# Kernel optimization log

Measured on AMD Instinct MI355X. Metric: run time of the kernel, lower is better.

Reference implementation:

```python
import jax, jax.numpy as jnp
import numpy as np

EPS = 1e-5
K = 3

def _bn(x, g, b):
    # training-mode BatchNorm2d: batch stats over (N,H,W), biased variance
    m = jnp.mean(x, axis=(0, 2, 3), keepdims=True)
    v = jnp.var(x, axis=(0, 2, 3), keepdims=True)
    return (x - m) * jax.lax.rsqrt(v + EPS) * g[None, :, None, None] + b[None, :, None, None]

def _gelu(x):
    return jax.nn.gelu(x, approximate=False)

def _dyn_dw(x, aw1, ab1, aw2, ab2):
    # dynamic depthwise conv: per-sample k^2 softmax weights shared over channels
    b, c, h, w = x.shape
    gap = jnp.mean(x, axis=(2, 3))                              # (b,c)
    h1 = jax.nn.relu(jnp.einsum('oc,bc->bo', aw1, gap) + ab1)   # (b,c//8)
    kw = jax.nn.softmax(jnp.einsum('oc,bc->bo', aw2, h1) + ab2, axis=1)  # (b,k^2)
    xp = jnp.pad(x, ((0, 0), (0, 0), (1, 1), (1, 1)))
    out = jnp.zeros_like(x)
    idx = 0
    for i in range(K):
        for j in range(K):
            out = out + kw[:, idx, None, None, None] * xp[:, :, i:i + h, j:j + w]
            idx += 1
    return out

def _channel_att(x, w1, w2):
    avg = jnp.mean(x, axis=(2, 3))        # (b,C)
    mx = jnp.max(x, axis=(2, 3))          # (b,C)
    def fc(v):
        return jnp.einsum('oc,bc->bo', w2, jax.nn.relu(jnp.einsum('oc,bc->bo', w1, v)))
    s = jax.nn.sigmoid(fc(avg) + fc(mx))  # (b,C)
    return s[:, :, None, None] * x

def _forward(x, w1, b1, g1, be1, aw1, ab1, aw2, ab2, g2, be2,
             ca_w1, ca_w2, pw, pb, g3, be3, sw, sb):
    b, n, d = x.shape
    h = w = int(np.sqrt(n))
    residual = x
    xi = jnp.transpose(x.reshape(b, h, w, d), (0, 3, 1, 2))       # (b,d,h,w)
    # pw_expand: 1x1 conv -> GELU -> BN
    y = jnp.einsum('oc,bchw->bohw', w1, xi) + b1[None, :, None, None]
    y = _bn(_gelu(y), g1, be1)                                    # (b,4d,h,w)
    # dw_conv: dynamic depthwise -> GELU -> BN -> channel attention
    y = _dyn_dw(y, aw1, ab1, aw2, ab2)
    y = _bn(_gelu(y), g2, be2)
    y = _channel_att(y, ca_w1, ca_w2)
    # spatial attention
    avg_o = jnp.mean(y, axis=1, keepdims=True)
    max_o = jnp.max(y, axis=1, keepdims=True)
    sp_in = jnp.concatenate([avg_o, max_o], axis=1)               # (b,2,h,w)
    sp = jax.lax.conv_general_dilated(sp_in, sw, (1, 1), ((3, 3), (3, 3)),
                                      dimension_numbers=('NCHW', 'OIHW', 'NCHW'))
    sp = jax.nn.sigmoid(sp + sb[None, :, None, None])
    y = y * sp
    # pw_project: 1x1 conv -> BN
    y = jnp.einsum('oc,bchw->bohw', pw, y) + pb[None, :, None, None]
    y = _bn(y, g3, be3)
    y = jnp.transpose(y, (0, 2, 3, 1)).reshape(b, n, d)
    return residual + y

def setup_inputs() -> dict:
    key = jax.random.key(0)
    ks = jax.random.split(key, 16)
    d, C = 256, 1024
    def rn(k, shape, fan):
        return jax.random.normal(k, shape, jnp.float32) * np.float32(np.sqrt(2.0 / fan))
    return {
        'x': jax.random.normal(ks[0], (8, 1024, d), jnp.float32),
        'w1': rn(ks[1], (C, d), d), 'b1': jnp.zeros((C,), jnp.float32),
        'g1': jnp.ones((C,), jnp.float32), 'be1': jnp.zeros((C,), jnp.float32),
        'aw1': rn(ks[2], (C // 8, C), C), 'ab1': jnp.zeros((C // 8,), jnp.float32),
        'aw2': rn(ks[3], (K * K, C // 8), C // 8), 'ab2': jnp.zeros((K * K,), jnp.float32),
        'g2': jnp.ones((C,), jnp.float32), 'be2': jnp.zeros((C,), jnp.float32),
        'ca_w1': rn(ks[4], (C // 16, C), C), 'ca_w2': rn(ks[5], (C, C // 16), C // 16),
        'pw': rn(ks[6], (d, C), C), 'pb': jnp.zeros((d,), jnp.float32),
        'g3': jnp.ones((d,), jnp.float32), 'be3': jnp.zeros((d,), jnp.float32),
        'sw': rn(ks[7], (1, 2, 7, 7), 2 * 49), 'sb': jnp.zeros((1,), jnp.float32),
    }

def reference(x, w1, b1, g1, be1, aw1, ab1, aw2, ab2, g2, be2,
              ca_w1, ca_w2, pw, pb, g3, be3, sw, sb):
    return _forward(x, w1, b1, g1, be1, aw1, ab1, aw2, ab2, g2, be2,
                    ca_w1, ca_w2, pw, pb, g3, be3, sw, sb)
```

## Files before the change

kernel.cpp:

```cpp
#include <hip/hip_runtime.h>
#include <math.h>

constexpr int B = 8;
constexpr int D = 256;
constexpr int C = 1024;
constexpr int H = 32, W = 32;
constexpr int P = H * W;
constexpr int M = B * P;
constexpr float EPS = 1e-5f;

typedef unsigned short u16;
typedef unsigned int u32;
typedef __attribute__((ext_vector_type(8))) short short8;
typedef __attribute__((ext_vector_type(4))) float floatx4;

constexpr size_t WS_CHSUM1 = 0;
constexpr size_t WS_CHSQ1  = 1024;
constexpr size_t WS_GAPSUM = 2048;
constexpr size_t WS_CHSUM3 = 10240;
constexpr size_t WS_CHSQ3  = 10496;
constexpr size_t WS_CHSUM2 = 10752;
constexpr size_t WS_CHSQ2  = 11776;
constexpr size_t WS_BSUM2  = 12800;
constexpr size_t WS_UMAX2  = 20992;
constexpr size_t WS_UMAXN2 = 29184;
constexpr size_t WS_ACC_COUNT = 37376;
constexpr size_t WS_SCALE1 = 37376;
constexpr size_t WS_SHIFT1 = 38400;
constexpr size_t WS_KW     = 39424;
constexpr size_t WS_SCALE2 = 39680;
constexpr size_t WS_SHIFT2 = 40704;
constexpr size_t WS_SATT   = 41728;
constexpr size_t WS_AVGO   = 49920;
constexpr size_t WS_MAXO   = 58112;
constexpr size_t WS_SP     = 66304;
constexpr size_t WS_PRE    = 74496;
constexpr size_t WS_T1B    = 2171648;
constexpr size_t WS_T2B    = 6365952;
constexpr size_t WS_XB     = 10560256;
constexpr size_t WS_W1B    = 11608832;
constexpr size_t WS_PWB    = 11739904;
constexpr size_t WS_YB     = 11870976;

__device__ __forceinline__ float gelu_exact(float v) {
    return 0.5f * v * (1.0f + erff(v * 0.70710678118654752440f));
}

__device__ __forceinline__ u16 f2bf(float f) {
    u32 u = __float_as_uint(f);
    u += 0x7fff + ((u >> 16) & 1);
    return (u16)(u >> 16);
}

__device__ __forceinline__ float bf2f(u16 v) {
    return __uint_as_float(((u32)v) << 16);
}

__device__ __forceinline__ u32 fkey(float f) {
    u32 u = __float_as_uint(f);
    return (u & 0x80000000u) ? ~u : (u | 0x80000000u);
}
__device__ __forceinline__ float fkeyinv(u32 k) {
    return __uint_as_float((k & 0x80000000u) ? (k ^ 0x80000000u) : ~k);
}

#define GLOAD(SRC, DST) __builtin_amdgcn_global_load_lds( \
    (const __attribute__((address_space(1))) void*)(SRC), \
    (__attribute__((address_space(3))) void*)(DST), 16, 0, 0)

__global__ __launch_bounds__(256) void cvt_all_kernel(const float* __restrict__ x,
                                                      const float* __restrict__ w1,
                                                      const float* __restrict__ pw,
                                                      u16* __restrict__ xb,
                                                      u16* __restrict__ w1b,
                                                      u16* __restrict__ pwb,
                                                      float* __restrict__ acc_zero) {
    const int i = blockIdx.x * 256 + threadIdx.x;
    if (i < (int)WS_ACC_COUNT) acc_zero[i] = 0.f;
    const float* src;
    u16* dst;
    int off;
    if (i < 524288)      { src = x;  dst = xb;  off = i; }
    else if (i < 589824) { src = w1; dst = w1b; off = i - 524288; }
    else                 { src = pw; dst = pwb; off = i - 589824; }
    const float4 v = *(const float4*)(src + (size_t)off * 4);
    uint2 o;
    o.x = ((u32)f2bf(v.x)) | ((u32)f2bf(v.y) << 16);
    o.y = ((u32)f2bf(v.z)) | ((u32)f2bf(v.w) << 16);
    *(uint2*)(dst + (size_t)off * 4) = o;
}

template<int KD, int EPI, int NS, int MB, int NB>
__global__ __launch_bounds__(256) void mfma_gemm_kernel(
    const u16* __restrict__ A,
    const u16* __restrict__ Bw,
    const float* __restrict__ bias,
    const float* __restrict__ rowscale,
    void* __restrict__ outv,
    float* __restrict__ csum,
    float* __restrict__ csq,
    float* __restrict__ gsum)
{
    constexpr int MI = MB / 32;
    constexpr int NJ = NB / 32;
    constexpr int ABUF = MB * 64;
    constexpr int BBUF = NB * 64;
    constexpr int GX = NS / NB;
    constexpr int NWG = (M / MB) * GX;
    constexpr int CPX = NWG / 8;
    extern __shared__ u16 smem[];
    u16* Ab0 = smem;
    u16* Ab1 = smem + ABUF;
    u16* Bb0 = smem + 2 * ABUF;
    u16* Bb1 = smem + 2 * ABUF + BBUF;
    const int t = threadIdx.x;
    const int lane = t & 63;

    const int lin = blockIdx.y * GX + blockIdx.x;
    const int swz = (lin & 7) * CPX + (lin >> 3);
    const int bx = swz % GX;
    const int by = swz / GX;
    const int row0 = by * MB;
    const int col0 = bx * NB;

    const int wv = t >> 6;
    const int wrow = (wv >> 1) * (MB / 2);
    const int wcol = (wv & 1) * (NB / 2);
    const int lm = lane & 15;
    const int lk8 = (lane >> 4) * 8;
    const int srow = t >> 2;
    const int scol = (t & 3) * 8;
    const u16* gA0 = A + (size_t)(row0 + srow) * KD + scol;
    const u16* gA1 = A + (size_t)(row0 + 64 + srow) * KD + scol;
    const u16* gB0 = Bw + (size_t)(col0 + srow) * KD + scol;
    const u16* gB1 = Bw + (size_t)(col0 + 64 + srow) * KD + scol;

    const floatx4 zero = {0.f, 0.f, 0.f, 0.f};
    floatx4 acc[MI][NJ];
#pragma unroll
    for (int i = 0; i < MI; ++i)
#pragma unroll
        for (int j = 0; j < NJ; ++j) acc[i][j] = zero;

    auto stage = [&](u16* As, u16* Bs, int k0) {
#pragma unroll
        for (int s2 = 0; s2 < 2; ++s2) {
            const int kk = k0 + s2 * 32;
            u16* Asub = As + s2 * (MB * 32);
            u16* Bsub = Bs + s2 * (NB * 32);
            GLOAD(gA0 + kk, Asub + t * 8);
            if constexpr (MB == 128) GLOAD(gA1 + kk, Asub + 2048 + t * 8);
            GLOAD(gB0 + kk, Bsub + t * 8);
            if constexpr (NB == 128) GLOAD(gB1 + kk, Bsub + 2048 + t * 8);
        }
    };
    auto compute = [&](const u16* As, const u16* Bs) {
#pragma unroll
        for (int s2 = 0; s2 < 2; ++s2) {
            const u16* Asub = As + s2 * (MB * 32);
            const u16* Bsub = Bs + s2 * (NB * 32);
            short8 af[MI], bf[NJ];
#pragma unroll
            for (int i = 0; i < MI; ++i)
                af[i] = *(const short8*)(Asub + (wrow + i * 16 + lm) * 32 + lk8);
#pragma unroll
            for (int j = 0; j < NJ; ++j)
                bf[j] = *(const short8*)(Bsub + (wcol + j * 16 + lm) * 32 + lk8);
#pragma unroll
            for (int i = 0; i < MI; ++i)
#pragma unroll
                for (int j = 0; j < NJ; ++j)
                    acc[i][j] = __builtin_amdgcn_mfma_f32_16x16x32_bf16(af[i], bf[j], acc[i][j], 0, 0, 0);
        }
    };

    stage(Ab0, Bb0, 0);
    __syncthreads();
    int cur = 0;
    for (int k0 = 0; k0 < KD; k0 += 64) {
        if (k0 + 64 < KD) stage(cur ? Ab0 : Ab1, cur ? Bb0 : Bb1, k0 + 64);
        compute(cur ? Ab1 : Ab0, cur ? Bb1 : Bb0);
        __syncthreads();
        cur ^= 1;
    }

    float colsum[NJ], colsq[NJ];
#pragma unroll
    for (int j = 0; j < NJ; ++j) { colsum[j] = 0.f; colsq[j] = 0.f; }

    if (EPI == 0) {
        u16* Cs = smem;
#pragma unroll
        for (int i = 0; i < MI; ++i) {
#pragma unroll
            for (int r = 0; r < 4; ++r) {
                const int lrow = wrow + i * 16 + (lane >> 4) * 4 + r;
#pragma unroll
                for (int j = 0; j < NJ; ++j) {
                    const int lcol = wcol + j * 16 + lm;
                    const float tv = gelu_exact(acc[i][j][r] + bias[col0 + lcol]);
                    Cs[lrow * NB + lcol] = f2bf(tv);
                    colsum[j] += tv;
                    colsq[j] = fmaf(tv, tv, colsq[j]);
                }
            }
        }
        __syncthreads();
        constexpr int TPR = NB / 8;
        constexpr int RPP = 256 / TPR;
        u16* outp = (u16*)outv;
#pragma unroll
        for (int p = 0; p < MB / RPP; ++p) {
            const int r = p * RPP + t / TPR;
            const int cc = (t % TPR) * 8;
            *(uint4*)(outp + (size_t)(row0 + r) * NS + col0 + cc) =
                *(const uint4*)(Cs + r * NB + cc);
        }
    } else {
        float* Cs = (float*)smem;
#pragma unroll
        for (int i = 0; i < MI; ++i) {
#pragma unroll
            for (int r = 0; r < 4; ++r) {
                const int lrow = wrow + i * 16 + (lane >> 4) * 4 + r;
                const float rs = rowscale[row0 + lrow];
#pragma unroll
                for (int j = 0; j < NJ; ++j) {
                    const int lcol = wcol + j * 16 + lm;
                    const float tv = rs * acc[i][j][r] + bias[col0 + lcol];
                    Cs[lrow * NB + lcol] = tv;
                    colsum[j] += tv;
                    colsq[j] = fmaf(tv, tv, colsq[j]);
                }
            }
        }
        __syncthreads();
        constexpr int TPR = NB / 4;
        constexpr int RPP = 256 / TPR;
        float* outp = (float*)outv;
#pragma unroll
        for (int p = 0; p < MB / RPP; ++p) {
            const int r = p * RPP + t / TPR;
            const int cc = (t % TPR) * 4;
            *(float4*)(outp + (size_t)(row0 + r) * NS + col0 + cc) =
                *(const float4*)(Cs + r * NB + cc);
        }
    }

    const int bb = (by * MB) >> 10;
#pragma unroll
    for (int j = 0; j < NJ; ++j) {
        float s = colsum[j];
        float q = colsq[j];
        s += __shfl_xor(s, 16); s += __shfl_xor(s, 32);
        q += __shfl_xor(q, 16); q += __shfl_xor(q, 32);
        if (lane < 16) {
            const int c = col0 + wcol + j * 16 + lm;
            atomicAdd(&csum[c], s);
            atomicAdd(&csq[c], q);
            if (EPI == 0) atomicAdd(&gsum[bb * NS + c], s);
        }
    }
}

__global__ __launch_bounds__(1024) void dynmlp_kernel(const float* __restrict__ chsum1,
                                                      const float* __restrict__ chsq1,
                                                      const float* __restrict__ gapsum,
                                                      const float* __restrict__ g1,
                                                      const float* __restrict__ be1,
                                                      const float* __restrict__ aw1,
                                                      const float* __restrict__ ab1,
                                                      const float* __restrict__ aw2,
                                                      const float* __restrict__ ab2,
                                                      float* __restrict__ scale1,
                                                      float* __restrict__ shift1,
                                                      float* __restrict__ kw) {
    const int b = blockIdx.x;
    const int t = threadIdx.x;
    const int wave = t >> 6, lane = t & 63;
    __shared__ float g[1024];
    __shared__ float h1[128];
    __shared__ float logits[12];
    {
        const float m = chsum1[t] * (1.0f / (float)M);
        const float var = chsq1[t] * (1.0f / (float)M) - m * m;
        const float rstd = rsqrtf(var + EPS);
        const float sc = rstd * g1[t];
        const float sh = be1[t] - m * sc;
        if (b == 0) { scale1[t] = sc; shift1[t] = sh; }
        g[t] = gapsum[b * C + t] * (1.0f / (float)P) * sc + sh;
    }
    __syncthreads();
#pragma unroll
    for (int k = 0; k < 8; ++k) {
        const int u = wave * 8 + k;
        const float4* wr = (const float4*)(aw1 + (size_t)u * C);
        float s = 0.f;
#pragma unroll
        for (int ch = 0; ch < 4; ++ch) {
            const float4 wv = wr[lane + 64 * ch];
            const float4 sv = *(const float4*)(g + 4 * lane + 256 * ch);
            s += wv.x * sv.x + wv.y * sv.y + wv.z * sv.z + wv.w * sv.w;
        }
#pragma unroll
        for (int off = 1; off < 64; off <<= 1) s += __shfl_xor(s, off);
        if (lane == 0) h1[u] = fmaxf(s + ab1[u], 0.f);
    }
    __syncthreads();
    if (wave < 9) {
        float s = aw2[wave * 128 + lane] * h1[lane]
                + aw2[wave * 128 + 64 + lane] * h1[64 + lane];
#pragma unroll
        for (int off = 1; off < 64; off <<= 1) s += __shfl_xor(s, off);
        if (lane == 0) logits[wave] = s + ab2[wave];
    }
    __syncthreads();
    if (t == 0) {
        float mx = logits[0];
        for (int i = 1; i < 9; ++i) mx = fmaxf(mx, logits[i]);
        float e[9], den = 0.f;
        for (int i = 0; i < 9; ++i) { e[i] = expf(logits[i] - mx); den += e[i]; }
        const float inv = 1.0f / den;
        for (int i = 0; i < 9; ++i) kw[b * 9 + i] = e[i] * inv;
    }
}

__global__ __launch_bounds__(256) void dwconv_kernel(const u16* __restrict__ t1b,
                                                     const float* __restrict__ scale1,
                                                     const float* __restrict__ shift1,
                                                     const float* __restrict__ kw,
                                                     u16* __restrict__ t2b,
                                                     float* __restrict__ chsum2,
                                                     float* __restrict__ chsq2,
                                                     float* __restrict__ bsum2,
                                                     u32* __restrict__ umax2,
                                                     u32* __restrict__ umaxn2) {
    __shared__ u16 rows[3 * 32 * 256];
    const int lin = blockIdx.y * 4 + blockIdx.x;
    const int swz = (lin & 7) * 128 + (lin >> 3);
    const int cq = swz & 3;
    const int bh = swz >> 2;
    const int b = bh >> 5;
    const int h = bh & 31;
    const int t = threadIdx.x;

    const u16* gbase = t1b + (size_t)b * P * C + cq * 256;
#pragma unroll
    for (int i = 0; i < 12; ++i) {
        const int lin2 = i * 256 + t;
        const int chunk = lin2 >> 5;
        const int r = chunk >> 5;
        const int w = chunk & 31;
        const int off8 = (lin2 & 31) * 8;
        const int hr = h + r - 1;
        uint4 v = {0u, 0u, 0u, 0u};
        if (hr >= 0 && hr < H)
            v = *(const uint4*)(gbase + (size_t)(hr * W + w) * C + off8);
        *(uint4*)(&rows[chunk * 256 + off8]) = v;
    }
    __syncthreads();

    const int c = t;
    const int gc = cq * 256 + c;
    float kk[9];
#pragma unroll
    for (int i = 0; i < 9; ++i) kk[i] = kw[b * 9 + i];
    const float sc = scale1[gc];
    const float sh = shift1[gc];
    float scm[3], shm[3];
    scm[0] = (h > 0)     ? sc : 0.f;  shm[0] = (h > 0)     ? sh : 0.f;
    scm[1] = sc;                      shm[1] = sh;
    scm[2] = (h < H - 1) ? sc : 0.f;  shm[2] = (h < H - 1) ? sh : 0.f;

    const u16* rp0 = rows + c;
#define DWVAL(ri, w) fmaf(bf2f(rp0[((ri) * 32 + (w)) * 256]), scm[ri], shm[ri])

    float vm0 = 0.f, vm1 = 0.f, vm2 = 0.f;
    float vc0 = DWVAL(0, 0), vc1 = DWVAL(1, 0), vc2 = DWVAL(2, 0);
    float vp0 = DWVAL(0, 1), vp1 = DWVAL(1, 1), vp2 = DWVAL(2, 1);

    float s = 0.f, q = 0.f, mx = -INFINITY, mn = INFINITY;
    u16* orow = t2b + ((size_t)b * P + h * W) * C + gc;
    for (int w = 0; w < W; ++w) {
        float acc;
        acc = kk[0] * vm0;
        acc = fmaf(kk[1], vc0, acc);
        acc = fmaf(kk[2], vp0, acc);
        acc = fmaf(kk[3], vm1, acc);
        acc = fmaf(kk[4], vc1, acc);
        acc = fmaf(kk[5], vp1, acc);
        acc = fmaf(kk[6], vm2, acc);
        acc = fmaf(kk[7], vc2, acc);
        acc = fmaf(kk[8], vp2, acc);
        const float y = gelu_exact(acc);
        orow[(size_t)w * C] = f2bf(y);
        s += y;
        q = fmaf(y, y, q);
        mx = fmaxf(mx, y);
        mn = fminf(mn, y);
        vm0 = vc0; vc0 = vp0;
        vm1 = vc1; vc1 = vp1;
        vm2 = vc2; vc2 = vp2;
        if (w + 2 < W) {
            vp0 = DWVAL(0, w + 2);
            vp1 = DWVAL(1, w + 2);
            vp2 = DWVAL(2, w + 2);
        } else {
            vp0 = 0.f; vp1 = 0.f; vp2 = 0.f;
        }
    }
#undef DWVAL
    atomicAdd(&chsum2[gc], s);
    atomicAdd(&chsq2[gc], q);
    atomicAdd(&bsum2[b * C + gc], s);
    atomicMax(&umax2[b * C + gc], fkey(mx));
    atomicMax(&umaxn2[b * C + gc], fkey(-mn));
}

__global__ __launch_bounds__(1024) void chatt_kernel(const float* __restrict__ chsum2,
                                                     const float* __restrict__ chsq2,
                                                     const float* __restrict__ bsum2,
                                                     const u32* __restrict__ umax2,
                                                     const u32* __restrict__ umaxn2,
                                                     const float* __restrict__ g2,
                                                     const float* __restrict__ be2,
                                                     const float* __restrict__ caw1,
                                                     const float* __restrict__ caw2,
                                                     float* __restrict__ scale2,
                                                     float* __restrict__ shift2,
                                                     float* __restrict__ s_att) {
    const int b = blockIdx.x;
    const int t = threadIdx.x;
    const int wave = t >> 6, lane = t & 63;
    __shared__ float la[1024], lx[1024], ha[64], hm[64];
    {
        const float m = chsum2[t] * (1.0f / (float)M);
        const float var = chsq2[t] * (1.0f / (float)M) - m * m;
        const float rstd = rsqrtf(var + EPS);
        const float sc = rstd * g2[t];
        const float sh = be2[t] - m * sc;
        if (b == 0) { scale2[t] = sc; shift2[t] = sh; }
        la[t] = bsum2[b * C + t] * (1.0f / (float)P) * sc + sh;
        const float mx = fkeyinv(umax2[b * C + t]);
        const float mn = -fkeyinv(umaxn2[b * C + t]);
        lx[t] = (sc >= 0.f ? mx : mn) * sc + sh;
    }
    __syncthreads();
#pragma unroll
    for (int k = 0; k < 8; ++k) {
        const int u = wave * 8 + k;
        const int row = u & 63;
        const float* src = (u < 64) ? la : lx;
        const float4* wr = (const float4*)(caw1 + (size_t)row * C);
        float s = 0.f;
#pragma unroll
        for (int ch = 0; ch < 4; ++ch) {
            const float4 wv = wr[lane + 64 * ch];
            const float4 sv = *(const float4*)(src + 4 * lane + 256 * ch);
            s += wv.x * sv.x + wv.y * sv.y + wv.z * sv.z + wv.w * sv.w;
        }
#pragma unroll
        for (int off = 1; off < 64; off <<= 1) s += __shfl_xor(s, off);
        if (lane == 0) {
            s = fmaxf(s, 0.f);
            if (u < 64) ha[row] = s; else hm[row] = s;
        }
    }
    __syncthreads();
    {
        const float4* w2 = (const float4*)(caw2 + (size_t)t * 64);
        float s = 0.f;
#pragma unroll
        for (int j = 0; j < 16; ++j) {
            const float4 wv = w2[j];
            s += wv.x * (ha[j * 4 + 0] + hm[j * 4 + 0]);
            s += wv.y * (ha[j * 4 + 1] + hm[j * 4 + 1]);
            s += wv.z * (ha[j * 4 + 2] + hm[j * 4 + 2]);
            s += wv.w * (ha[j * 4 + 3] + hm[j * 4 + 3]);
        }
        s_att[b * C + t] = 1.0f / (1.0f + expf(-s));
    }
}

__global__ __launch_bounds__(256) void yq_kernel(const u16* __restrict__ t2b,
                                                 const float* __restrict__ scale2,
                                                 const float* __restrict__ shift2,
                                                 const float* __restrict__ s_att,
                                                 u16* __restrict__ yb,
                                                 float* __restrict__ avg_o,
                                                 float* __restrict__ max_o) {
    const int row = blockIdx.x;
    const int b = row >> 10;
    const int t = threadIdx.x;
    const int c0 = t * 4;
    const uint2 vv = *(const uint2*)(t2b + (size_t)row * C + c0);
    const float v0 = bf2f((u16)(vv.x & 0xffff));
    const float v1 = bf2f((u16)(vv.x >> 16));
    const float v2 = bf2f((u16)(vv.y & 0xffff));
    const float v3 = bf2f((u16)(vv.y >> 16));
    const float4 sc = *(const float4*)(scale2 + c0);
    const float4 sh = *(const float4*)(shift2 + c0);
    const float4 sa = *(const float4*)(s_att + (size_t)b * C + c0);
    const float y0 = fmaf(v0, sc.x, sh.x) * sa.x;
    const float y1 = fmaf(v1, sc.y, sh.y) * sa.y;
    const float y2 = fmaf(v2, sc.z, sh.z) * sa.z;
    const float y3 = fmaf(v3, sc.w, sh.w) * sa.w;
    uint2 o;
    o.x = ((u32)f2bf(y0)) | ((u32)f2bf(y1) << 16);
    o.y = ((u32)f2bf(y2)) | ((u32)f2bf(y3) << 16);
    *(uint2*)(yb + (size_t)row * C + c0) = o;
    float s = (y0 + y1) + (y2 + y3);
    float mx = fmaxf(fmaxf(y0, y1), fmaxf(y2, y3));
#pragma unroll
    for (int off = 32; off > 0; off >>= 1) {
        s += __shfl_down(s, off);
        mx = fmaxf(mx, __shfl_down(mx, off));
    }
    __shared__ float ss[4], sm[4];
    const int wave = t >> 6, lane = t & 63;
    if (lane == 0) { ss[wave] = s; sm[wave] = mx; }
    __syncthreads();
    if (t == 0) {
        const float S = ss[0] + ss[1] + ss[2] + ss[3];
        const float Mx = fmaxf(fmaxf(sm[0], sm[1]), fmaxf(sm[2], sm[3]));
        avg_o[row] = S * (1.0f / (float)C);
        max_o[row] = Mx;
    }
}

__global__ __launch_bounds__(1024) void spconv_kernel(const float* __restrict__ avg_o,
                                                      const float* __restrict__ max_o,
                                                      const float* __restrict__ sw,
                                                      const float* __restrict__ sb,
                                                      float* __restrict__ sp) {
    const int b = blockIdx.x;
    const int t = threadIdx.x;
    __shared__ float pa[P], pm[P], wsh[98];
    pa[t] = avg_o[b * P + t];
    pm[t] = max_o[b * P + t];
    if (t < 98) wsh[t] = sw[t];
    const float sbv = sb[0];
    __syncthreads();
    const int h = t >> 5, w = t & 31;
    float acc = sbv;
#pragma unroll
    for (int i = 0; i < 7; ++i) {
        const int hh = h + i - 3;
        if (hh < 0 || hh >= H) continue;
#pragma unroll
        for (int j = 0; j < 7; ++j) {
            const int ww = w + j - 3;
            if (ww < 0 || ww >= W) continue;
            const int pidx = hh * W + ww;
            acc = fmaf(wsh[i * 7 + j], pa[pidx], acc);
            acc = fmaf(wsh[49 + i * 7 + j], pm[pidx], acc);
        }
    }
    sp[b * P + t] = 1.0f / (1.0f + expf(-acc));
}

__global__ __launch_bounds__(256) void final_kernel(const float* __restrict__ x,
                                                    const float* __restrict__ pre,
                                                    const float* __restrict__ chsum3,
                                                    const float* __restrict__ chsq3,
                                                    const float* __restrict__ g3,
                                                    const float* __restrict__ be3,
                                                    float* __restrict__ out) {
    __shared__ float lsc[256], lsh[256];
    const int t = threadIdx.x;
    {
        const float m = chsum3[t] * (1.0f / (float)M);
        const float var = chsq3[t] * (1.0f / (float)M) - m * m;
        const float rstd = rsqrtf(var + EPS);
        const float sc = rstd * g3[t];
        lsc[t] = sc;
        lsh[t] = be3[t] - m * sc;
    }
    __syncthreads();
    const int i = blockIdx.x * 256 + t;
    const int e = i * 4;
    const int d = e & 255;
    const float4 xv = *(const float4*)(x + e);
    const float4 pv = *(const float4*)(pre + e);
    const float4 sc = *(const float4*)(lsc + d);
    const float4 sh = *(const float4*)(lsh + d);
    float4 o;
    o.x = xv.x + fmaf(pv.x, sc.x, sh.x);
    o.y = xv.y + fmaf(pv.y, sc.y, sh.y);
    o.z = xv.z + fmaf(pv.z, sc.z, sh.z);
    o.w = xv.w + fmaf(pv.w, sc.w, sh.w);
    *(float4*)(out + e) = o;
}

extern "C" void kernel_launch(void* const* d_in, const int* in_sizes, int n_in,
                              void* d_out, int out_size, void* d_ws, size_t ws_size,
                              hipStream_t stream) {
    const float* x    = (const float*)d_in[0];
    const float* w1   = (const float*)d_in[1];
    const float* b1   = (const float*)d_in[2];
    const float* g1   = (const float*)d_in[3];
    const float* be1  = (const float*)d_in[4];
    const float* aw1  = (const float*)d_in[5];
    const float* ab1  = (const float*)d_in[6];
    const float* aw2  = (const float*)d_in[7];
    const float* ab2  = (const float*)d_in[8];
    const float* g2   = (const float*)d_in[9];
    const float* be2  = (const float*)d_in[10];
    const float* caw1 = (const float*)d_in[11];
    const float* caw2 = (const float*)d_in[12];
    const float* pw   = (const float*)d_in[13];
    const float* pb   = (const float*)d_in[14];
    const float* g3   = (const float*)d_in[15];
    const float* be3  = (const float*)d_in[16];
    const float* sw   = (const float*)d_in[17];
    const float* sb   = (const float*)d_in[18];
    float* out = (float*)d_out;
    float* ws = (float*)d_ws;

    float* chsum1  = ws + WS_CHSUM1;
    float* chsq1   = ws + WS_CHSQ1;
    float* gapsum  = ws + WS_GAPSUM;
    float* chsum3  = ws + WS_CHSUM3;
    float* chsq3   = ws + WS_CHSQ3;
    float* chsum2  = ws + WS_CHSUM2;
    float* chsq2   = ws + WS_CHSQ2;
    float* bsum2   = ws + WS_BSUM2;
    u32*   umax2   = (u32*)(ws + WS_UMAX2);
    u32*   umaxn2  = (u32*)(ws + WS_UMAXN2);
    float* scale1  = ws + WS_SCALE1;
    float* shift1  = ws + WS_SHIFT1;
    float* kw      = ws + WS_KW;
    float* scale2  = ws + WS_SCALE2;
    float* shift2  = ws + WS_SHIFT2;
    float* s_att   = ws + WS_SATT;
    float* avg_o   = ws + WS_AVGO;
    float* max_o   = ws + WS_MAXO;
    float* sp      = ws + WS_SP;
    float* pre     = ws + WS_PRE;
    u16* t1b = (u16*)(ws + WS_T1B);
    u16* t2b = (u16*)(ws + WS_T2B);
    u16* xb  = (u16*)(ws + WS_XB);
    u16* w1b = (u16*)(ws + WS_W1B);
    u16* pwb = (u16*)(ws + WS_PWB);
    u16* yb  = (u16*)(ws + WS_YB);

    cvt_all_kernel<<<dim3(2560), 256, 0, stream>>>(x, w1, pw, xb, w1b, pwb, ws);
    mfma_gemm_kernel<256, 0, C, 128, 128><<<dim3(C / 128, M / 128), 256, 65536, stream>>>(
        xb, w1b, b1, nullptr, t1b, chsum1, chsq1, gapsum);
    dynmlp_kernel<<<dim3(B), 1024, 0, stream>>>(chsum1, chsq1, gapsum, g1, be1,
                                                aw1, ab1, aw2, ab2, scale1, shift1, kw);
    dwconv_kernel<<<dim3(4, B * H), 256, 0, stream>>>(t1b, scale1, shift1, kw, t2b,
                                                      chsum2, chsq2, bsum2, umax2, umaxn2);
    chatt_kernel<<<dim3(B), 1024, 0, stream>>>(chsum2, chsq2, bsum2, umax2, umaxn2,
                                               g2, be2, caw1, caw2, scale2, shift2, s_att);
    yq_kernel<<<dim3(M), 256, 0, stream>>>(t2b, scale2, shift2, s_att, yb, avg_o, max_o);
    spconv_kernel<<<dim3(B), 1024, 0, stream>>>(avg_o, max_o, sw, sb, sp);
    mfma_gemm_kernel<1024, 1, D, 64, 64><<<dim3(D / 64, M / 64), 256, 32768, stream>>>(
        yb, pwb, pb, sp, pre, chsum3, chsq3, nullptr);
    final_kernel<<<dim3((M * D / 4) / 256), 256, 0, stream>>>(x, pre, chsum3, chsq3, g3, be3, out);
}
```

Measured before the change: 207.4 us.

## Rework MFMA GEMM pipeline to 32-wide K chunks with vmcnt waits and smaller tiles

The GEMM main loop now stages 32-wide K chunks into a double buffer and uses explicit s_waitcnt vmcnt and raw s_barrier calls in place of __syncthreads, so the next chunk's global-to-LDS loads stay in flight while the current chunk is computed. The first GEMM moves from 128x128 to 128x64 tiles, and both GEMMs ask for less LDS, which should let more workgroups run per CU. The risks are more barriers per K step, less reuse per tile, and a fragile dependence on the hand-written vmcnt counts matching the number of issued loads.

Result: faster. 202.8 us (-2.3%).

```diff
diff --git a/kernel.cpp b/kernel.cpp
--- a/kernel.cpp
+++ b/kernel.cpp
@@ -103,16 +103,17 @@
 {
     constexpr int MI = MB / 32;
     constexpr int NJ = NB / 32;
-    constexpr int ABUF = MB * 64;
-    constexpr int BBUF = NB * 64;
+    constexpr int ABUF = MB * 32;
+    constexpr int BBUF = NB * 32;
+    constexpr int BUFSZ = ABUF + BBUF;
+    constexpr int GA = MB / 64;
+    constexpr int GB = NB / 64;
+    constexpr int LD = GA + GB;
+    constexpr int NCH = KD / 32;
     constexpr int GX = NS / NB;
     constexpr int NWG = (M / MB) * GX;
     constexpr int CPX = NWG / 8;
     extern __shared__ u16 smem[];
-    u16* Ab0 = smem;
-    u16* Ab1 = smem + ABUF;
-    u16* Bb0 = smem + 2 * ABUF;
-    u16* Bb1 = smem + 2 * ABUF + BBUF;
     const int t = threadIdx.x;
     const int lane = t & 63;
 
@@ -130,10 +131,8 @@
     const int lk8 = (lane >> 4) * 8;
     const int srow = t >> 2;
     const int scol = (t & 3) * 8;
-    const u16* gA0 = A + (size_t)(row0 + srow) * KD + scol;
-    const u16* gA1 = A + (size_t)(row0 + 64 + srow) * KD + scol;
-    const u16* gB0 = Bw + (size_t)(col0 + srow) * KD + scol;
-    const u16* gB1 = Bw + (size_t)(col0 + 64 + srow) * KD + scol;
+    const u16* gA = A + (size_t)(row0 + srow) * KD + scol;
+    const u16* gB = Bw + (size_t)(col0 + srow) * KD + scol;
 
     const floatx4 zero = {0.f, 0.f, 0.f, 0.f};
     floatx4 acc[MI][NJ];
@@ -142,46 +141,48 @@
 #pragma unroll
         for (int j = 0; j < NJ; ++j) acc[i][j] = zero;
 
-    auto stage = [&](u16* As, u16* Bs, int k0) {
-#pragma unroll
-        for (int s2 = 0; s2 < 2; ++s2) {
-            const int kk = k0 + s2 * 32;
-            u16* Asub = As + s2 * (MB * 32);
-            u16* Bsub = Bs + s2 * (NB * 32);
-            GLOAD(gA0 + kk, Asub + t * 8);
-            if constexpr (MB == 128) GLOAD(gA1 + kk, Asub + 2048 + t * 8);
-            GLOAD(gB0 + kk, Bsub + t * 8);
-            if constexpr (NB == 128) GLOAD(gB1 + kk, Bsub + 2048 + t * 8);
-        }
+    auto stage = [&](u16* buf, int c) {
+        const int kk = c * 32;
+        u16* As = buf;
+        u16* Bs = buf + ABUF;
+#pragma unroll
+        for (int g = 0; g < GA; ++g)
+            GLOAD(gA + (size_t)g * 64 * KD + kk, As + g * 2048 + t * 8);
+#pragma unroll
+        for (int g = 0; g < GB; ++g)
+            GLOAD(gB + (size_t)g * 64 * KD + kk, Bs + g * 2048 + t * 8);
     };
-    auto compute = [&](const u16* As, const u16* Bs) {
-#pragma unroll
-        for (int s2 = 0; s2 < 2; ++s2) {
-            const u16* Asub = As + s2 * (MB * 32);
-            const u16* Bsub = Bs + s2 * (NB * 32);
-            short8 af[MI], bf[NJ];
-#pragma unroll
-            for (int i = 0; i < MI; ++i)
-                af[i] = *(const short8*)(Asub + (wrow + i * 16 + lm) * 32 + lk8);
+    auto compute = [&](const u16* buf) {
+        const u16* As = buf;
+        const u16* Bs = buf + ABUF;
+        short8 af[MI], bf[NJ];
+#pragma unroll
+        for (int i = 0; i < MI; ++i)
+            af[i] = *(const short8*)(As + (wrow + i * 16 + lm) * 32 + lk8);
+#pragma unroll
+        for (int j = 0; j < NJ; ++j)
+            bf[j] = *(const short8*)(Bs + (wcol + j * 16 + lm) * 32 + lk8);
+#pragma unroll
+        for (int i = 0; i < MI; ++i)
 #pragma unroll
             for (int j = 0; j < NJ; ++j)
-                bf[j] = *(const short8*)(Bsub + (wcol + j * 16 + lm) * 32 + lk8);
-#pragma unroll
-            for (int i = 0; i < MI; ++i)
-#pragma unroll
-                for (int j = 0; j < NJ; ++j)
-                    acc[i][j] = __builtin_amdgcn_mfma_f32_16x16x32_bf16(af[i], bf[j], acc[i][j], 0, 0, 0);
-        }
+                acc[i][j] = __builtin_amdgcn_mfma_f32_16x16x32_bf16(af[i], bf[j], acc[i][j], 0, 0, 0);
     };
 
-    stage(Ab0, Bb0, 0);
-    __syncthreads();
-    int cur = 0;
-    for (int k0 = 0; k0 < KD; k0 += 64) {
-        if (k0 + 64 < KD) stage(cur ? Ab0 : Ab1, cur ? Bb0 : Bb1, k0 + 64);
-        compute(cur ? Ab1 : Ab0, cur ? Bb1 : Bb0);
-        __syncthreads();
-        cur ^= 1;
+    stage(smem, 0);
+    for (int c = 0; c < NCH; ++c) {
+        u16* curb = smem + (c & 1) * BUFSZ;
+        if (c + 1 < NCH) {
+            stage(smem + ((c + 1) & 1) * BUFSZ, c + 1);
+            if constexpr (LD == 2) asm volatile("s_waitcnt vmcnt(2)" ::: "memory");
+            else                   asm volatile("s_waitcnt vmcnt(3)" ::: "memory");
+        } else {
+            asm volatile("s_waitcnt vmcnt(0)" ::: "memory");
+        }
+        __builtin_amdgcn_s_barrier();
+        compute(curb);
+        asm volatile("s_waitcnt lgkmcnt(0)" ::: "memory");
+        __builtin_amdgcn_s_barrier();
     }
 
     float colsum[NJ], colsq[NJ];
@@ -645,7 +646,7 @@
     u16* yb  = (u16*)(ws + WS_YB);
 
     cvt_all_kernel<<<dim3(2560), 256, 0, stream>>>(x, w1, pw, xb, w1b, pwb, ws);
-    mfma_gemm_kernel<256, 0, C, 128, 128><<<dim3(C / 128, M / 128), 256, 65536, stream>>>(
+    mfma_gemm_kernel<256, 0, C, 128, 64><<<dim3(C / 64, M / 128), 256, 24576, stream>>>(
         xb, w1b, b1, nullptr, t1b, chsum1, chsq1, gapsum);
     dynmlp_kernel<<<dim3(B), 1024, 0, stream>>>(chsum1, chsq1, gapsum, g1, be1,
                                                 aw1, ab1, aw2, ab2, scale1, shift1, kw);
@@ -655,7 +656,7 @@
                                                g2, be2, caw1, caw2, scale2, shift2, s_att);
     yq_kernel<<<dim3(M), 256, 0, stream>>>(t2b, scale2, shift2, s_att, yb, avg_o, max_o);
     spconv_kernel<<<dim3(B), 1024, 0, stream>>>(avg_o, max_o, sw, sb, sp);
-    mfma_gemm_kernel<1024, 1, D, 64, 64><<<dim3(D / 64, M / 64), 256, 32768, stream>>>(
+    mfma_gemm_kernel<1024, 1, D, 64, 64><<<dim3(D / 64, M / 64), 256, 16384, stream>>>(
         yb, pwb, pb, sp, pre, chsum3, chsq3, nullptr);
     final_kernel<<<dim3((M * D / 4) / 256), 256, 0, stream>>>(x, pre, chsum3, chsq3, g3, be3, out);
 }
```
